# Kernel optimization log

Measured on AMD Instinct MI355X. Metric: run time of the kernel, lower is better.

## Reference

```python
import jax, jax.numpy as jnp
import numpy as np
from jax import lax

WS = 8            # window size
N = WS * WS       # tokens per window
NH = 8            # num heads
DIM = 256
HD = DIM // NH    # head dim


def _rel_tables():
    # continuous relative coords table, [1, 2*WS-1, 2*WS-1, 2]
    c = np.arange(-(WS - 1), WS, dtype=np.float32)
    table = np.stack(np.meshgrid(c, c, indexing='ij'), axis=-1)[None]
    table = table / (WS - 1) * 8.0
    table = np.sign(table) * np.log2(np.abs(table) + 1.0) / np.log2(8.0)
    # relative position index, [N, N] int
    coords = np.stack(np.meshgrid(np.arange(WS), np.arange(WS), indexing='ij'))
    cf = coords.reshape(2, -1)
    rel = (cf[:, :, None] - cf[:, None, :]).transpose(1, 2, 0)  # [N, N, 2]
    rel[..., 0] += WS - 1
    rel[..., 1] += WS - 1
    rel[..., 0] *= 2 * WS - 1
    idx = rel.sum(-1)
    return jnp.asarray(table, jnp.float32), jnp.asarray(idx, jnp.int32)


def setup_inputs() -> dict:
    key = jax.random.key(0)
    ks = jax.random.split(key, 12)
    s = 0.02
    return {
        'x': jax.random.normal(ks[0], (8, DIM, 128, 128), jnp.float32),
        'qkv_w': jax.random.normal(ks[1], (3 * DIM, DIM), jnp.float32) * s,
        'qkv_b': jax.random.normal(ks[2], (3 * DIM,), jnp.float32) * s,
        'proj_w': jax.random.normal(ks[3], (DIM, DIM), jnp.float32) * s,
        'proj_b': jax.random.normal(ks[4], (DIM,), jnp.float32) * s,
        'pe_w': jax.random.normal(ks[5], (DIM, 1, 3, 3), jnp.float32) * s,
        'pe_b': jax.random.normal(ks[6], (DIM,), jnp.float32) * s,
        'logit_scale': jnp.full((NH, 1, 1), np.log(10.0), jnp.float32),
        'cpb_w1': jax.random.normal(ks[7], (DIM, 2), jnp.float32) * s,
        'cpb_b1': jax.random.normal(ks[8], (DIM,), jnp.float32) * s,
        'cpb_w2': jax.random.normal(ks[9], (NH, DIM), jnp.float32) * s,
    }


def _conv1x1(x, w, b):
    # fused conv1x1 + eval-mode BN: [B,Ci,H,W] x [Co,Ci] -> [B,Co,H,W]
    return jnp.einsum('bchw,oc->bohw', x, w) + b[None, :, None, None]


def _window_partition(x):
    # [B,C,H,W] -> [B*nWh*nWw, N, C]; H,W divisible by WS (reflect pad no-op)
    B, C, H, W = x.shape
    x = x.reshape(B, C, H // WS, WS, W // WS, WS)
    x = x.transpose(0, 2, 4, 3, 5, 1)  # [B, nWh, nWw, ws, ws, C]
    return x.reshape(-1, N, C)


def _window_reverse(wins, B, H, W, C):
    # [B*nWh*nWw, N, C] -> [B, C, H, W]
    t = wins.reshape(B, H // WS, W // WS, WS, WS, C)
    t = t.transpose(0, 5, 1, 3, 2, 4)
    return t.reshape(B, C, H, W)


def reference(x, qkv_w, qkv_b, proj_w, proj_b, pe_w, pe_b,
              logit_scale, cpb_w1, cpb_b1, cpb_w2):
    B, C, H, W = x.shape
    table, idx = _rel_tables()

    qkv = _conv1x1(x, qkv_w, qkv_b)                      # [B, 3C, H, W]
    qkv_w_ = _window_partition(qkv)                      # [B_, N, 3C]
    B_ = qkv_w_.shape[0]
    qkv_w_ = qkv_w_.reshape(B_, N, NH, 3 * HD).transpose(0, 2, 1, 3)
    q, k, v = jnp.split(qkv_w_, 3, axis=-1)              # each [B_, NH, N, HD]

    qn = q / jnp.maximum(jnp.linalg.norm(q, axis=-1, keepdims=True), 1e-12)
    kn = k / jnp.maximum(jnp.linalg.norm(k, axis=-1, keepdims=True), 1e-12)
    attn = jnp.einsum('bhnd,bhmd->bhnm', qn, kn)         # cosine sim
    ls = jnp.exp(jnp.minimum(logit_scale, jnp.log(jnp.float32(100.0))))
    attn = attn * ls[None]                               # [B_, NH, N, N]

    # CPB MLP -> relative position bias gather
    h1 = jax.nn.relu(jnp.einsum('qtwc,dc->qtwd', table, cpb_w1) + cpb_b1)
    bias_table = jnp.einsum('qtwd,hd->qtwh', h1, cpb_w2).reshape(-1, NH)
    bias = bias_table[idx.reshape(-1)].reshape(N, N, NH).transpose(2, 0, 1)
    bias = 16.0 * jax.nn.sigmoid(bias)                   # [NH, N, N]

    attn = jax.nn.softmax(attn + bias[None], axis=-1)

    out = jnp.einsum('bhnm,bhmd->bhnd', attn, v)         # [B_, NH, N, HD]
    out = out.transpose(0, 2, 1, 3).reshape(B_, N, C)
    out_img = _window_reverse(out, B, H, W, C)           # [B, C, H, W]

    v_img = _window_reverse(v.transpose(0, 2, 1, 3).reshape(B_, N, C), B, H, W, C)
    pe = lax.conv_general_dilated(
        v_img, pe_w, (1, 1), 'SAME',
        dimension_numbers=('NCHW', 'OIHW', 'NCHW'),
        feature_group_count=C) + pe_b[None, :, None, None]

    return _conv1x1(out_img + pe, proj_w, proj_b)
```

## Files before the change

kernel.cpp:

```cpp
#include <hip/hip_runtime.h>

typedef unsigned short u16;
typedef unsigned int u32;
typedef short bf16x8 __attribute__((ext_vector_type(8)));
typedef float f32x4 __attribute__((ext_vector_type(4)));
typedef unsigned short u16x8 __attribute__((ext_vector_type(8)));
typedef unsigned short u16x4 __attribute__((ext_vector_type(4)));

#define DEVFN static __device__ __forceinline__

DEVFN u16 f2b(float f) {
    u32 u = __builtin_bit_cast(u32, f);
    u += 0x7FFFu + ((u >> 16) & 1u);
    return (u16)(u >> 16);
}
DEVFN float b2f(u16 h) {
    u32 u = ((u32)h) << 16;
    return __builtin_bit_cast(float, u);
}

typedef const __attribute__((address_space(1))) unsigned int glb_u32;
typedef __attribute__((address_space(3))) unsigned int lds_u32;
DEVFN void gload_lds16(const u16* g, u16* l) {
    __builtin_amdgcn_global_load_lds((glb_u32*)g, (lds_u32*)l, 16, 0, 0);
}

__global__ void k_prep(const float* __restrict__ qkvw, const float* __restrict__ pjw,
                       u16* __restrict__ qkvwb, u16* __restrict__ pjwb) {
    int id = blockIdx.x * 256 + threadIdx.x;
    if (id < 196608) qkvwb[id] = f2b(qkvw[id]);
    if (id < 65536)  pjwb[id]  = f2b(pjw[id]);
}

__global__ void k_cpb(const float* __restrict__ w1, const float* __restrict__ b1,
                      const float* __restrict__ w2, float* __restrict__ bt) {
    int p = threadIdx.x;
    if (p >= 225) return;
    int d0 = p / 15, d1 = p % 15;
    float v0 = (float)(d0 - 7) * (8.0f / 7.0f);
    float v1 = (float)(d1 - 7) * (8.0f / 7.0f);
    float t0 = copysignf(log2f(fabsf(v0) + 1.0f) * (1.0f / 3.0f), v0);
    float t1 = copysignf(log2f(fabsf(v1) + 1.0f) * (1.0f / 3.0f), v1);
    float s[8] = {0.f, 0.f, 0.f, 0.f, 0.f, 0.f, 0.f, 0.f};
    for (int d = 0; d < 256; ++d) {
        float h = t0 * w1[2 * d] + t1 * w1[2 * d + 1] + b1[d];
        h = fmaxf(h, 0.0f);
        #pragma unroll
        for (int hh = 0; hh < 8; ++hh) s[hh] += h * w2[hh * 256 + d];
    }
    #pragma unroll
    for (int hh = 0; hh < 8; ++hh) bt[p * 8 + hh] = s[hh];
}

__global__ void k_bias(const float* __restrict__ bt, float* __restrict__ biasT) {
    int id = blockIdx.x * 256 + threadIdx.x;
    int kq = id >> 6, q = id & 63;
    int d0 = (q >> 3) - (kq >> 3) + 7;
    int d1 = (q & 7) - (kq & 7) + 7;
    int p = d0 * 15 + d1;
    #pragma unroll
    for (int h = 0; h < 8; ++h)
        biasT[h * 4096 + id] = 16.0f / (1.0f + expf(-bt[p * 8 + h]));
}

__global__ __launch_bounds__(256) void k_xcvt(const float* __restrict__ x,
                                              u16* __restrict__ xt) {
    const int bid = blockIdx.x;
    const int xcd = bid & 7;
    const int i = bid >> 3;
    const int rowblk = xcd * 128 + (i >> 2);
    const int c = i & 3;
    const int tid = threadIdx.x;
    const int g = tid & 7;
    const int tseg = tid >> 3;
    const int tok0 = tseg * 4;
    const float* src = x + ((size_t)(rowblk >> 7) * 256 + c * 64 + g * 8) * 16384
                         + (rowblk & 127) * 128 + tok0;
    float4 v[8];
    #pragma unroll
    for (int j = 0; j < 8; ++j)
        v[j] = *(const float4*)(src + (size_t)j * 16384);
    u16x8 o0, o1, o2, o3;
    #pragma unroll
    for (int j = 0; j < 8; ++j) {
        o0[j] = f2b(v[j].x);
        o1[j] = f2b(v[j].y);
        o2[j] = f2b(v[j].z);
        o3[j] = f2b(v[j].w);
    }
    const int s0 = g ^ ((tseg ^ (tok0 + 0)) & 7);
    const int s1 = g ^ ((tseg ^ (tok0 + 1)) & 7);
    const int s2 = g ^ ((tseg ^ (tok0 + 2)) & 7);
    const int s3 = g ^ ((tseg ^ (tok0 + 3)) & 7);
    u16* dst = xt + ((size_t)rowblk * 4 + c) * 8192;
    *(u16x8*)&dst[(tok0 + 0) * 64 + (s0 << 3)] = o0;
    *(u16x8*)&dst[(tok0 + 1) * 64 + (s1 << 3)] = o1;
    *(u16x8*)&dst[(tok0 + 2) * 64 + (s2 << 3)] = o2;
    *(u16x8*)&dst[(tok0 + 3) * 64 + (s3 << 3)] = o3;
}

__global__ __launch_bounds__(256, 3) void k_qkv(
    const u16* __restrict__ xt, const u16* __restrict__ qkvw,
    const float* __restrict__ qkvb,
    u16* __restrict__ gq, u16* __restrict__ gk, u16* __restrict__ wv_g) {
    __shared__ __align__(16) u16 Xs[2][8192];

    const int bid = blockIdx.x;
    const int xcd = bid & 7;
    const int idx = bid >> 3;
    const int ny = idx % 6;
    const int rowblk = xcd * 128 + idx / 6;
    const int b = rowblk >> 7, row = rowblk & 127;
    const int which = ny >> 1, half = ny & 1;

    const int tid = threadIdx.x;
    const int wave = tid >> 6, l = tid & 63, col = l & 15, quad = l >> 4;
    const int th = wave >> 1;
    const int oq = wave & 1;
    const int obase = half * 128 + oq * 64;

    int orow[4];
    #pragma unroll
    for (int nt = 0; nt < 4; ++nt) {
        const int oo = obase + nt * 16 + col;
        orow[nt] = (oo >> 5) * 96 + which * 32 + (oo & 31);
    }

    f32x4 acc[4][4];
    #pragma unroll
    for (int i = 0; i < 4; ++i)
        #pragma unroll
        for (int j = 0; j < 4; ++j) acc[i][j] = f32x4{0.f, 0.f, 0.f, 0.f};

    const u16* xtb = xt + (size_t)rowblk * 32768;

    auto stage = [&](int c, int buf) {
        const u16* src = xtb + c * 8192 + wave * 2048 + l * 8;
        u16* dst = &Xs[buf][wave * 2048];
        #pragma unroll
        for (int i = 0; i < 4; ++i)
            gload_lds16(src + i * 512, dst + i * 512);
    };
    auto loadW = [&](int c, bf16x8* bw) {
        #pragma unroll
        for (int kk = 0; kk < 2; ++kk)
            #pragma unroll
            for (int nt = 0; nt < 4; ++nt)
                bw[kk * 4 + nt] = *(const bf16x8*)&qkvw[(size_t)orow[nt] * 256 +
                                                        c * 64 + kk * 32 + quad * 8];
    };
    auto gemm = [&](int buf, const bf16x8* bw) {
        #pragma unroll
        for (int kk = 0; kk < 2; ++kk) {
            const int lchunk = kk * 4 + quad;
            bf16x8 af[4];
            #pragma unroll
            for (int mt = 0; mt < 4; ++mt) {
                const int tok = th * 64 + mt * 16 + col;
                const int slot = lchunk ^ (((tok >> 2) ^ tok) & 7);
                af[mt] = *(const bf16x8*)&Xs[buf][tok * 64 + (slot << 3)];
            }
            #pragma unroll
            for (int nt = 0; nt < 4; ++nt)
                #pragma unroll
                for (int mt = 0; mt < 4; ++mt)
                    acc[nt][mt] = __builtin_amdgcn_mfma_f32_16x16x32_bf16(
                        bw[kk * 4 + nt], af[mt], acc[nt][mt], 0, 0, 0);
        }
    };

    bf16x8 bwA[8], bwB[8];
    stage(0, 0);
    loadW(0, bwA);
    __syncthreads();
    #pragma unroll
    for (int c = 0; c < 4; ++c) {
        if (c < 3) {
            stage(c + 1, (c + 1) & 1);
            loadW(c + 1, (c & 1) ? bwA : bwB);
        }
        gemm(c & 1, (c & 1) ? bwB : bwA);
        __syncthreads();
    }

    const int hA = obase >> 5;
    f32x4 bqv[4];
    #pragma unroll
    for (int nt = 0; nt < 4; ++nt) {
        const int oo = obase + nt * 16 + quad * 4;
        bqv[nt] = *(const f32x4*)&qkvb[(oo >> 5) * 96 + which * 32 + (oo & 31)];
    }
    #pragma unroll
    for (int mt = 0; mt < 4; ++mt) {
        const int tok = th * 64 + mt * 16 + col;
        const int win = b * 256 + (row >> 3) * 16 + (tok >> 3);
        const int tk = (row & 7) * 8 + (tok & 7);
        float v[4][4];
        #pragma unroll
        for (int nt = 0; nt < 4; ++nt)
            #pragma unroll
            for (int r = 0; r < 4; ++r)
                v[nt][r] = acc[nt][mt][r] + bqv[nt][r];
        if (which < 2) {
            float sA = 0.f, sB = 0.f;
            #pragma unroll
            for (int r = 0; r < 4; ++r) {
                sA += v[0][r] * v[0][r] + v[1][r] * v[1][r];
                sB += v[2][r] * v[2][r] + v[3][r] * v[3][r];
            }
            sA += __shfl_xor(sA, 16, 64);
            sA += __shfl_xor(sA, 32, 64);
            sB += __shfl_xor(sB, 16, 64);
            sB += __shfl_xor(sB, 32, 64);
            const float iA = 1.0f / fmaxf(sqrtf(sA), 1e-12f);
            const float iB = 1.0f / fmaxf(sqrtf(sB), 1e-12f);
            #pragma unroll
            for (int r = 0; r < 4; ++r) {
                v[0][r] *= iA; v[1][r] *= iA;
                v[2][r] *= iB; v[3][r] *= iB;
            }
        }
        #pragma unroll
        for (int nt = 0; nt < 4; ++nt) {
            u16x4 ov;
            #pragma unroll
            for (int r = 0; r < 4; ++r) ov[r] = f2b(v[nt][r]);
            if (which == 2) {
                *(u16x4*)&wv_g[((size_t)win * 64 + tk) * 256 + obase + nt * 16 + quad * 4] = ov;
            } else {
                u16* G = (which == 0) ? gq : gk;
                const int h = hA + (nt >> 1);
                const int d = (nt & 1) * 16 + quad * 4;
                *(u16x4*)&G[((size_t)(win * 8 + h) * 64 + tk) * 32 + d] = ov;
            }
        }
    }
}

__global__ __launch_bounds__(256, 3) void k_attn3(
    const u16* __restrict__ gq, const u16* __restrict__ gk,
    const u16* __restrict__ wv_g,
    const float* __restrict__ lsc, const float* __restrict__ biasT,
    u16* __restrict__ wout_g) {
    __shared__ __align__(16) u16 scr[4][2048];

    const int tid = threadIdx.x;
    const int wave = tid >> 6, l = tid & 63, col = l & 15, quad = l >> 4;
    const int bid = blockIdx.x;
    const int xcd = bid & 7;
    const int jl = (bid >> 3) * 4 + wave;
    const int h = jl >> 8;
    const int win = xcd * 256 + (jl & 255);
    u16* const v_t = scr[wave];

    #pragma unroll
    for (int it = 0; it < 4; ++it) {
        const int idx = it * 64 + l;
        const int tok = idx & 63, dblk = idx >> 6;
        const u16x8 vv = *(const u16x8*)&wv_g[((size_t)win * 64 + tok) * 256 + h * 32 + dblk * 8];
        const int g = (tok >> 5) * 4 + ((tok >> 2) & 3);
        const int jj = ((tok >> 4) & 1) * 4 + (tok & 3);
        #pragma unroll
        for (int j = 0; j < 8; ++j) {
            const int d = dblk * 8 + j;
            v_t[d * 64 + (((g ^ (d & 7)) << 3) | jj)] = vv[j];
        }
    }

    const u16* const qbp = gq + (size_t)(win * 8 + h) * 2048;
    const u16* const kbp = gk + (size_t)(win * 8 + h) * 2048;
    bf16x8 ak[4], bq[4];
    #pragma unroll
    for (int mt = 0; mt < 4; ++mt)
        ak[mt] = *(const bf16x8*)&kbp[(mt * 16 + col) * 32 + quad * 8];
    #pragma unroll
    for (int nt = 0; nt < 4; ++nt)
        bq[nt] = *(const bf16x8*)&qbp[(nt * 16 + col) * 32 + quad * 8];

    const f32x4 zero4 = {0.f, 0.f, 0.f, 0.f};
    f32x4 sacc[4][4];
    #pragma unroll
    for (int mt = 0; mt < 4; ++mt)
        #pragma unroll
        for (int nt = 0; nt < 4; ++nt)
            sacc[mt][nt] = __builtin_amdgcn_mfma_f32_16x16x32_bf16(ak[mt], bq[nt], zero4, 0, 0, 0);

    const float ls = expf(fminf(lsc[h], 4.6051701859880914f));
    const float* bT = biasT + h * 4096;
    #pragma unroll
    for (int nt = 0; nt < 4; ++nt) {
        const int q = nt * 16 + col;
        float v[4][4];
        float mx = -1e30f;
        #pragma unroll
        for (int mt = 0; mt < 4; ++mt)
            #pragma unroll
            for (int r = 0; r < 4; ++r) {
                v[mt][r] = sacc[mt][nt][r] * ls + bT[(mt * 16 + quad * 4 + r) * 64 + q];
                mx = fmaxf(mx, v[mt][r]);
            }
        mx = fmaxf(mx, __shfl_xor(mx, 16, 64));
        mx = fmaxf(mx, __shfl_xor(mx, 32, 64));
        float s = 0.f;
        #pragma unroll
        for (int mt = 0; mt < 4; ++mt)
            #pragma unroll
            for (int r = 0; r < 4; ++r) {
                v[mt][r] = expf(v[mt][r] - mx);
                s += v[mt][r];
            }
        s += __shfl_xor(s, 16, 64);
        s += __shfl_xor(s, 32, 64);
        const float inv = 1.0f / s;
        #pragma unroll
        for (int mt = 0; mt < 4; ++mt)
            #pragma unroll
            for (int r = 0; r < 4; ++r)
                sacc[mt][nt][r] = v[mt][r] * inv;
    }

    f32x4 oacc[2][4];
    #pragma unroll
    for (int i = 0; i < 2; ++i)
        #pragma unroll
        for (int j = 0; j < 4; ++j) oacc[i][j] = zero4;
    #pragma unroll
    for (int kk = 0; kk < 2; ++kk) {
        bf16x8 av[2];
        #pragma unroll
        for (int dt = 0; dt < 2; ++dt) {
            const int d = dt * 16 + col;
            av[dt] = *(const bf16x8*)&v_t[d * 64 + (((kk * 4 + quad) ^ (d & 7)) << 3)];
        }
        #pragma unroll
        for (int nt = 0; nt < 4; ++nt) {
            union { u16x8 u; bf16x8 b; } pk;
            #pragma unroll
            for (int j = 0; j < 4; ++j) {
                pk.u[j]     = f2b(sacc[kk * 2][nt][j]);
                pk.u[j + 4] = f2b(sacc[kk * 2 + 1][nt][j]);
            }
            #pragma unroll
            for (int dt = 0; dt < 2; ++dt)
                oacc[dt][nt] = __builtin_amdgcn_mfma_f32_16x16x32_bf16(
                    av[dt], pk.b, oacc[dt][nt], 0, 0, 0);
        }
    }
    #pragma unroll
    for (int dt = 0; dt < 2; ++dt)
        #pragma unroll
        for (int qt = 0; qt < 4; ++qt) {
            const int t = qt * 16 + col;
            u16x4 ov;
            #pragma unroll
            for (int r = 0; r < 4; ++r) ov[r] = f2b(oacc[dt][qt][r]);
            *(u16x4*)&wout_g[((size_t)win * 64 + t) * 256 + h * 32 + dt * 16 + quad * 4] = ov;
        }
}

__global__ __launch_bounds__(256, 4) void k_proj(
    const u16* __restrict__ wout_g, const u16* __restrict__ wv_g,
    const float* __restrict__ pe_w, const float* __restrict__ pe_b,
    const u16* __restrict__ pjw, const float* __restrict__ pjb,
    float* __restrict__ out) {
    __shared__ __align__(16) u16 y_s[64 * 256];
    const int bid0 = blockIdx.x;
    const int win = (bid0 & 7) * 256 + (bid0 >> 3);
    const int b = win >> 8;
    const int h0 = ((win >> 4) & 15) * 8;
    const int w0 = (win & 15) * 8;
    const int tid = threadIdx.x;
    const int cg = tid & 31, ch = cg * 8;
    const int psub = tid >> 5;

    float pw[9][8];
    #pragma unroll
    for (int j = 0; j < 8; ++j)
        #pragma unroll
        for (int k = 0; k < 9; ++k) pw[k][j] = pe_w[(ch + j) * 9 + k];
    float pb[8];
    #pragma unroll
    for (int j = 0; j < 8; ++j) pb[j] = pe_b[ch + j];

    for (int it = 0; it < 8; ++it) {
        const int p = it * 8 + psub;
        const int gh = h0 + (p >> 3), gw = w0 + (p & 7);
        float a[8];
        {
            const bf16x8 ov = *(const bf16x8*)&wout_g[((size_t)win * 64 + p) * 256 + ch];
            #pragma unroll
            for (int j = 0; j < 8; ++j) a[j] = b2f((u16)ov[j]) + pb[j];
        }
        #pragma unroll
        for (int dy = -1; dy <= 1; ++dy)
            #pragma unroll
            for (int dx = -1; dx <= 1; ++dx) {
                const int hh = gh + dy, ww2 = gw + dx;
                if (hh < 0 || hh >= 128 || ww2 < 0 || ww2 >= 128) continue;
                const int nwin = b * 256 + (hh >> 3) * 16 + (ww2 >> 3);
                const int ntk = (hh & 7) * 8 + (ww2 & 7);
                const bf16x8 vv = *(const bf16x8*)&wv_g[((size_t)nwin * 64 + ntk) * 256 + ch];
                const int k = (dy + 1) * 3 + (dx + 1);
                #pragma unroll
                for (int j = 0; j < 8; ++j) a[j] += b2f((u16)vv[j]) * pw[k][j];
            }
        u16x8 tmp;
        #pragma unroll
        for (int j = 0; j < 8; ++j) tmp[j] = f2b(a[j]);
        *(u16x8*)&y_s[p * 256 + (((ch >> 3) ^ (p & 7)) << 3)] = tmp;
    }
    __syncthreads();

    const int wave = tid >> 6, l = tid & 63;
    const int col = l & 15, quad = l >> 4;
    const f32x4 zero4 = {0.f, 0.f, 0.f, 0.f};
    f32x4 macc[4][4];
    #pragma unroll
    for (int pt = 0; pt < 4; ++pt)
        #pragma unroll
        for (int ot = 0; ot < 4; ++ot) macc[pt][ot] = zero4;
    const int ob = wave * 64;
    for (int kk = 0; kk < 8; ++kk) {
        const int cb = kk * 32 + quad * 8;
        bf16x8 aw[4], by[4];
        #pragma unroll
        for (int ot = 0; ot < 4; ++ot)
            aw[ot] = *(const bf16x8*)&pjw[(size_t)(ob + ot * 16 + col) * 256 + cb];
        #pragma unroll
        for (int pt = 0; pt < 4; ++pt) {
            const int p = pt * 16 + col;
            by[pt] = *(const bf16x8*)&y_s[p * 256 + (((cb >> 3) ^ (p & 7)) << 3)];
        }
        #pragma unroll
        for (int pt = 0; pt < 4; ++pt)
            #pragma unroll
            for (int ot = 0; ot < 4; ++ot)
                macc[pt][ot] = __builtin_amdgcn_mfma_f32_16x16x32_bf16(
                    by[pt], aw[ot], macc[pt][ot], 0, 0, 0);
    }
    #pragma unroll
    for (int ot = 0; ot < 4; ++ot) {
        const int o = ob + ot * 16 + col;
        const float pbv = pjb[o];
        #pragma unroll
        for (int pt = 0; pt < 4; ++pt) {
            const int p0 = pt * 16 + quad * 4;
            float4 ov;
            ov.x = macc[pt][ot][0] + pbv;
            ov.y = macc[pt][ot][1] + pbv;
            ov.z = macc[pt][ot][2] + pbv;
            ov.w = macc[pt][ot][3] + pbv;
            *(float4*)&out[((size_t)(b * 256 + o)) * 16384 +
                           (h0 + (p0 >> 3)) * 128 + w0 + (p0 & 7)] = ov;
        }
    }
}

extern "C" void kernel_launch(void* const* d_in, const int* in_sizes, int n_in,
                              void* d_out, int out_size, void* d_ws, size_t ws_size,
                              hipStream_t stream) {
    const float* x    = (const float*)d_in[0];
    const float* qkvw = (const float*)d_in[1];
    const float* qkvb = (const float*)d_in[2];
    const float* pjw  = (const float*)d_in[3];
    const float* pjb  = (const float*)d_in[4];
    const float* pew  = (const float*)d_in[5];
    const float* peb  = (const float*)d_in[6];
    const float* lsc  = (const float*)d_in[7];
    const float* w1   = (const float*)d_in[8];
    const float* b1   = (const float*)d_in[9];
    const float* w2   = (const float*)d_in[10];

    char* ws = (char*)d_ws;
    u16* wv_b    = (u16*)(ws);
    u16* wout_b  = (u16*)(ws + (64ull << 20));
    u16* qkvwb   = (u16*)(ws + (128ull << 20));
    u16* pjwb    = (u16*)(ws + (128ull << 20) + 393216);
    float* biasT = (float*)(ws + (128ull << 20) + 393216 + 131072);
    float* bt    = (float*)(ws + (128ull << 20) + 393216 + 262144);

    u16* xt = wout_b;
    u16* gq = (u16*)d_out;
    u16* gk = gq + 33554432u;

    hipLaunchKernelGGL(k_prep, dim3(768), dim3(256), 0, stream, qkvw, pjw, qkvwb, pjwb);
    hipLaunchKernelGGL(k_cpb,  dim3(1),   dim3(256), 0, stream, w1, b1, w2, bt);
    hipLaunchKernelGGL(k_bias, dim3(16),  dim3(256), 0, stream, bt, biasT);
    hipLaunchKernelGGL(k_xcvt, dim3(4096), dim3(256), 0, stream, x, xt);
    hipLaunchKernelGGL(k_qkv,  dim3(6144), dim3(256), 0, stream,
                       xt, qkvwb, qkvb, gq, gk, wv_b);
    hipLaunchKernelGGL(k_attn3, dim3(4096), dim3(256), 0, stream,
                       gq, gk, wv_b, lsc, biasT, wout_b);
    hipLaunchKernelGGL(k_proj, dim3(2048), dim3(256), 0, stream,
                       wout_b, wv_b, pew, peb, pjwb, pjb, (float*)d_out);
}
```

Baseline: 387.3 us.

## Load full X row-block once per block and loop over q/k/v outputs

The QKV kernel now has each 512-thread block load the entire 128-token by 256-channel activation tile into LDS once, then loop over the three q/k/v output groups, each wave covering 64 outputs. Before, six blocks each re-streamed the same X tile in double-buffered chunks. This removes the redundant X reloads and the per-chunk barriers. In exchange the grid shrinks from 6144 to 1024 blocks, LDS per block grows to 64 KB, and the three output groups run serially with no load/compute overlap.

Result: slower. 459.8 us (+18.7%).

```diff
diff --git a/kernel.cpp b/kernel.cpp
--- a/kernel.cpp
+++ b/kernel.cpp
@@ -99,139 +99,131 @@
     *(u16x8*)&dst[(tok0 + 3) * 64 + (s3 << 3)] = o3;
 }
 
-__global__ __launch_bounds__(256, 3) void k_qkv(
+__global__ __launch_bounds__(512, 2) void k_qkv(
     const u16* __restrict__ xt, const u16* __restrict__ qkvw,
     const float* __restrict__ qkvb,
     u16* __restrict__ gq, u16* __restrict__ gk, u16* __restrict__ wv_g) {
-    __shared__ __align__(16) u16 Xs[2][8192];
+    __shared__ __align__(16) u16 Xs[4 * 8192];
 
     const int bid = blockIdx.x;
-    const int xcd = bid & 7;
-    const int idx = bid >> 3;
-    const int ny = idx % 6;
-    const int rowblk = xcd * 128 + idx / 6;
+    const int rowblk = (bid & 7) * 128 + (bid >> 3);
     const int b = rowblk >> 7, row = rowblk & 127;
-    const int which = ny >> 1, half = ny & 1;
 
     const int tid = threadIdx.x;
     const int wave = tid >> 6, l = tid & 63, col = l & 15, quad = l >> 4;
-    const int th = wave >> 1;
-    const int oq = wave & 1;
-    const int obase = half * 128 + oq * 64;
-
-    int orow[4];
-    #pragma unroll
-    for (int nt = 0; nt < 4; ++nt) {
-        const int oo = obase + nt * 16 + col;
-        orow[nt] = (oo >> 5) * 96 + which * 32 + (oo & 31);
-    }
-
-    f32x4 acc[4][4];
-    #pragma unroll
-    for (int i = 0; i < 4; ++i)
-        #pragma unroll
-        for (int j = 0; j < 4; ++j) acc[i][j] = f32x4{0.f, 0.f, 0.f, 0.f};
-
-    const u16* xtb = xt + (size_t)rowblk * 32768;
-
-    auto stage = [&](int c, int buf) {
-        const u16* src = xtb + c * 8192 + wave * 2048 + l * 8;
-        u16* dst = &Xs[buf][wave * 2048];
+    const int th = (wave >> 2) * 64;
+    const int obase = (wave & 3) * 64;
+
+    {
+        const u16* src = xt + (size_t)rowblk * 32768 + wave * 4096 + l * 8;
+        u16* dst = &Xs[wave * 4096];
+        #pragma unroll
+        for (int i = 0; i < 8; ++i)
+            gload_lds16(src + i * 512, dst + i * 512);
+    }
+    __syncthreads();
+
+    #pragma unroll 1
+    for (int which = 0; which < 3; ++which) {
+        int orow[4];
+        #pragma unroll
+        for (int nt = 0; nt < 4; ++nt) {
+            const int oo = obase + nt * 16 + col;
+            orow[nt] = (oo >> 5) * 96 + which * 32 + (oo & 31);
+        }
+
+        f32x4 acc[4][4];
         #pragma unroll
         for (int i = 0; i < 4; ++i)
-            gload_lds16(src + i * 512, dst + i * 512);
-    };
-    auto loadW = [&](int c, bf16x8* bw) {
-        #pragma unroll
-        for (int kk = 0; kk < 2; ++kk)
+            #pragma unroll
+            for (int j = 0; j < 4; ++j) acc[i][j] = f32x4{0.f, 0.f, 0.f, 0.f};
+
+        auto loadW = [&](int c, bf16x8* bw) {
+            #pragma unroll
+            for (int kk = 0; kk < 2; ++kk)
+                #pragma unroll
+                for (int nt = 0; nt < 4; ++nt)
+                    bw[kk * 4 + nt] = *(const bf16x8*)&qkvw[(size_t)orow[nt] * 256 +
+                                                            c * 64 + kk * 32 + quad * 8];
+        };
+        auto gemm = [&](int c, const bf16x8* bw) {
+            #pragma unroll
+            for (int kk = 0; kk < 2; ++kk) {
+                const int lchunk = kk * 4 + quad;
+                bf16x8 af[4];
+                #pragma unroll
+                for (int mt = 0; mt < 4; ++mt) {
+                    const int tok = th + mt * 16 + col;
+                    const int slot = lchunk ^ (((tok >> 2) ^ tok) & 7);
+                    af[mt] = *(const bf16x8*)&Xs[c * 8192 + tok * 64 + (slot << 3)];
+                }
+                #pragma unroll
+                for (int nt = 0; nt < 4; ++nt)
+                    #pragma unroll
+                    for (int mt = 0; mt < 4; ++mt)
+                        acc[nt][mt] = __builtin_amdgcn_mfma_f32_16x16x32_bf16(
+                            bw[kk * 4 + nt], af[mt], acc[nt][mt], 0, 0, 0);
+            }
+        };
+
+        bf16x8 bwA[8], bwB[8];
+        loadW(0, bwA);
+        #pragma unroll
+        for (int c = 0; c < 4; ++c) {
+            if (c < 3) loadW(c + 1, (c & 1) ? bwA : bwB);
+            gemm(c, (c & 1) ? bwB : bwA);
+        }
+
+        const int hA = obase >> 5;
+        f32x4 bqv[4];
+        #pragma unroll
+        for (int nt = 0; nt < 4; ++nt) {
+            const int oo = obase + nt * 16 + quad * 4;
+            bqv[nt] = *(const f32x4*)&qkvb[(oo >> 5) * 96 + which * 32 + (oo & 31)];
+        }
+        #pragma unroll
+        for (int mt = 0; mt < 4; ++mt) {
+            const int tok = th + mt * 16 + col;
+            const int win = b * 256 + (row >> 3) * 16 + (tok >> 3);
+            const int tk = (row & 7) * 8 + (tok & 7);
+            float v[4][4];
             #pragma unroll
             for (int nt = 0; nt < 4; ++nt)
-                bw[kk * 4 + nt] = *(const bf16x8*)&qkvw[(size_t)orow[nt] * 256 +
-                                                        c * 64 + kk * 32 + quad * 8];
-    };
-    auto gemm = [&](int buf, const bf16x8* bw) {
-        #pragma unroll
-        for (int kk = 0; kk < 2; ++kk) {
-            const int lchunk = kk * 4 + quad;
-            bf16x8 af[4];
-            #pragma unroll
-            for (int mt = 0; mt < 4; ++mt) {
-                const int tok = th * 64 + mt * 16 + col;
-                const int slot = lchunk ^ (((tok >> 2) ^ tok) & 7);
-                af[mt] = *(const bf16x8*)&Xs[buf][tok * 64 + (slot << 3)];
-            }
-            #pragma unroll
-            for (int nt = 0; nt < 4; ++nt)
-                #pragma unroll
-                for (int mt = 0; mt < 4; ++mt)
-                    acc[nt][mt] = __builtin_amdgcn_mfma_f32_16x16x32_bf16(
-                        bw[kk * 4 + nt], af[mt], acc[nt][mt], 0, 0, 0);
-        }
-    };
-
-    bf16x8 bwA[8], bwB[8];
-    stage(0, 0);
-    loadW(0, bwA);
-    __syncthreads();
-    #pragma unroll
-    for (int c = 0; c < 4; ++c) {
-        if (c < 3) {
-            stage(c + 1, (c + 1) & 1);
-            loadW(c + 1, (c & 1) ? bwA : bwB);
-        }
-        gemm(c & 1, (c & 1) ? bwB : bwA);
-        __syncthreads();
-    }
-
-    const int hA = obase >> 5;
-    f32x4 bqv[4];
-    #pragma unroll
-    for (int nt = 0; nt < 4; ++nt) {
-        const int oo = obase + nt * 16 + quad * 4;
-        bqv[nt] = *(const f32x4*)&qkvb[(oo >> 5) * 96 + which * 32 + (oo & 31)];
-    }
-    #pragma unroll
-    for (int mt = 0; mt < 4; ++mt) {
-        const int tok = th * 64 + mt * 16 + col;
-        const int win = b * 256 + (row >> 3) * 16 + (tok >> 3);
-        const int tk = (row & 7) * 8 + (tok & 7);
-        float v[4][4];
-        #pragma unroll
-        for (int nt = 0; nt < 4; ++nt)
-            #pragma unroll
-            for (int r = 0; r < 4; ++r)
-                v[nt][r] = acc[nt][mt][r] + bqv[nt][r];
-        if (which < 2) {
-            float sA = 0.f, sB = 0.f;
-            #pragma unroll
-            for (int r = 0; r < 4; ++r) {
-                sA += v[0][r] * v[0][r] + v[1][r] * v[1][r];
-                sB += v[2][r] * v[2][r] + v[3][r] * v[3][r];
-            }
-            sA += __shfl_xor(sA, 16, 64);
-            sA += __shfl_xor(sA, 32, 64);
-            sB += __shfl_xor(sB, 16, 64);
-            sB += __shfl_xor(sB, 32, 64);
-            const float iA = 1.0f / fmaxf(sqrtf(sA), 1e-12f);
-            const float iB = 1.0f / fmaxf(sqrtf(sB), 1e-12f);
-            #pragma unroll
-            for (int r = 0; r < 4; ++r) {
-                v[0][r] *= iA; v[1][r] *= iA;
-                v[2][r] *= iB; v[3][r] *= iB;
-            }
-        }
-        #pragma unroll
-        for (int nt = 0; nt < 4; ++nt) {
-            u16x4 ov;
-            #pragma unroll
-            for (int r = 0; r < 4; ++r) ov[r] = f2b(v[nt][r]);
-            if (which == 2) {
-                *(u16x4*)&wv_g[((size_t)win * 64 + tk) * 256 + obase + nt * 16 + quad * 4] = ov;
-            } else {
-                u16* G = (which == 0) ? gq : gk;
-                const int h = hA + (nt >> 1);
-                const int d = (nt & 1) * 16 + quad * 4;
-                *(u16x4*)&G[((size_t)(win * 8 + h) * 64 + tk) * 32 + d] = ov;
+                #pragma unroll
+                for (int r = 0; r < 4; ++r)
+                    v[nt][r] = acc[nt][mt][r] + bqv[nt][r];
+            if (which < 2) {
+                float sA = 0.f, sB = 0.f;
+                #pragma unroll
+                for (int r = 0; r < 4; ++r) {
+                    sA += v[0][r] * v[0][r] + v[1][r] * v[1][r];
+                    sB += v[2][r] * v[2][r] + v[3][r] * v[3][r];
+                }
+                sA += __shfl_xor(sA, 16, 64);
+                sA += __shfl_xor(sA, 32, 64);
+                sB += __shfl_xor(sB, 16, 64);
+                sB += __shfl_xor(sB, 32, 64);
+                const float iA = 1.0f / fmaxf(sqrtf(sA), 1e-12f);
+                const float iB = 1.0f / fmaxf(sqrtf(sB), 1e-12f);
+                #pragma unroll
+                for (int r = 0; r < 4; ++r) {
+                    v[0][r] *= iA; v[1][r] *= iA;
+                    v[2][r] *= iB; v[3][r] *= iB;
+                }
+            }
+            #pragma unroll
+            for (int nt = 0; nt < 4; ++nt) {
+                u16x4 ov;
+                #pragma unroll
+                for (int r = 0; r < 4; ++r) ov[r] = f2b(v[nt][r]);
+                if (which == 2) {
+                    *(u16x4*)&wv_g[((size_t)win * 64 + tk) * 256 + obase + nt * 16 + quad * 4] = ov;
+                } else {
+                    u16* G = (which == 0) ? gq : gk;
+                    const int h = hA + (nt >> 1);
+                    const int d = (nt & 1) * 16 + quad * 4;
+                    *(u16x4*)&G[((size_t)(win * 8 + h) * 64 + tk) * 32 + d] = ov;
+                }
             }
         }
     }
@@ -487,7 +479,7 @@
     hipLaunchKernelGGL(k_cpb,  dim3(1),   dim3(256), 0, stream, w1, b1, w2, bt);
     hipLaunchKernelGGL(k_bias, dim3(16),  dim3(256), 0, stream, bt, biasT);
     hipLaunchKernelGGL(k_xcvt, dim3(4096), dim3(256), 0, stream, x, xt);
-    hipLaunchKernelGGL(k_qkv,  dim3(6144), dim3(256), 0, stream,
+    hipLaunchKernelGGL(k_qkv,  dim3(1024), dim3(512), 0, stream,
                        xt, qkvwb, qkvb, gq, gk, wv_b);
     hipLaunchKernelGGL(k_attn3, dim3(4096), dim3(256), 0, stream,
                        gq, gk, wv_b, lsc, biasT, wout_b);
```
